# Optimization experiments

Measured on AMD Instinct MI355X. Metric: run time of the kernel, lower is better.

The kernel has to match this reference:

```python
import jax, jax.numpy as jnp
import numpy as np

HIDDEN = 2048
N_HEADS = 32
N_KV_HEADS = 8
HEAD_DIM = HIDDEN // N_HEADS  # 64
GROUPS = N_HEADS // N_KV_HEADS  # 4
ROPE_THETA = 10000.0
B, S = 1, 2048


def setup_inputs() -> dict:
    key = jax.random.key(0)
    ks = jax.random.split(key, 5)
    scale = 1.0 / np.sqrt(HIDDEN)
    return {
        "hidden_states": jax.random.normal(ks[0], (B, S, HIDDEN), dtype=jnp.float32),
        "Wq": jax.random.normal(ks[1], (HIDDEN, N_HEADS * HEAD_DIM), dtype=jnp.float32) * scale,
        "Wk": jax.random.normal(ks[2], (HIDDEN, N_KV_HEADS * HEAD_DIM), dtype=jnp.float32) * scale,
        "Wv": jax.random.normal(ks[3], (HIDDEN, N_KV_HEADS * HEAD_DIM), dtype=jnp.float32) * scale,
        "Wo": jax.random.normal(ks[4], (N_HEADS * HEAD_DIM, HIDDEN), dtype=jnp.float32) * scale,
    }


def _rope_tables(seq_len, dtype):
    # freqs_cos/sin buffers: [seq_len, HEAD_DIM//2]
    inv_freq = 1.0 / (ROPE_THETA ** (jnp.arange(0, HEAD_DIM, 2, dtype=jnp.float32) / HEAD_DIM))
    t = jnp.arange(seq_len, dtype=jnp.float32)
    freqs = jnp.outer(t, inv_freq)
    return jnp.cos(freqs).astype(dtype), jnp.sin(freqs).astype(dtype)


def _apply_rope(x, cos, sin):
    # x: [B, H, S, Dh], interleaved even/odd rotation
    xe = x[..., 0::2]
    xo = x[..., 1::2]
    # cos/sin: [S, Dh/2] -> broadcast over batch & heads
    out_e = xe * cos - xo * sin
    out_o = xe * sin + xo * cos
    return jnp.stack([out_e, out_o], axis=-1).reshape(x.shape)


def reference(hidden_states, Wq, Wk, Wv, Wo):
    bsz, q_len, _ = hidden_states.shape
    dtype = hidden_states.dtype

    q = (hidden_states @ Wq).reshape(bsz, q_len, N_HEADS, HEAD_DIM).transpose(0, 2, 1, 3)
    k = (hidden_states @ Wk).reshape(bsz, q_len, N_KV_HEADS, HEAD_DIM).transpose(0, 2, 1, 3)
    v = (hidden_states @ Wv).reshape(bsz, q_len, N_KV_HEADS, HEAD_DIM).transpose(0, 2, 1, 3)

    cos, sin = _rope_tables(q_len, dtype)
    q = _apply_rope(q, cos, sin)
    k = _apply_rope(k, cos, sin)

    # GQA: repeat_interleave kv heads to match query heads
    k = jnp.repeat(k, GROUPS, axis=1)  # [B, H, S, Dh]
    v = jnp.repeat(v, GROUPS, axis=1)

    # attention_mask=None path: no mask applied (matches module default)
    scores = jnp.einsum("bhqd,bhkd->bhqk", q, k) / jnp.sqrt(jnp.asarray(HEAD_DIM, dtype))
    attn = jax.nn.softmax(scores.astype(jnp.float32), axis=-1).astype(dtype)
    out = jnp.einsum("bhqk,bhkd->bhqd", attn, v)
    out = out.transpose(0, 2, 1, 3).reshape(bsz, q_len, N_HEADS * HEAD_DIM)
    return out @ Wo
```

## Files before the change

### kernel.cpp

```cpp
#include <hip/hip_runtime.h>

typedef __bf16 bf16x8 __attribute__((ext_vector_type(8)));
typedef float f32x4 __attribute__((ext_vector_type(4)));
typedef unsigned short u16x4 __attribute__((ext_vector_type(4)));
typedef unsigned short u16x8 __attribute__((ext_vector_type(8)));
typedef unsigned int u32x4 __attribute__((ext_vector_type(4)));

__device__ __forceinline__ float bf2f(unsigned short h) {
    union { unsigned int u; float f; } v;
    v.u = ((unsigned int)h) << 16;
    return v.f;
}
__device__ __forceinline__ unsigned short f2bf(float f) {
    return __builtin_bit_cast(unsigned short, (__bf16)f);
}
__device__ __forceinline__ void glds16(const unsigned short* g, unsigned short* l) {
    __builtin_amdgcn_global_load_lds((__attribute__((address_space(1))) void*)g,
                                     (__attribute__((address_space(3))) void*)l,
                                     16, 0, 0);
}

#define MFMA16(a, b, c) __builtin_amdgcn_mfma_f32_16x16x32_bf16((a), (b), (c), 0, 0, 0)

__global__ __launch_bounds__(256) void cvt_f32_bf16(const float* __restrict__ src,
                                                    unsigned short* __restrict__ dst) {
    const int i = (blockIdx.x * 256 + threadIdx.x) * 4;
    const float4 v = *(const float4*)(src + i);
    u16x4 o;
    o[0] = f2bf(v.x); o[1] = f2bf(v.y); o[2] = f2bf(v.z); o[3] = f2bf(v.w);
    *(u16x4*)(dst + i) = o;
}

__global__ __launch_bounds__(256) void cvt_transpose_wqkv(const float* __restrict__ Wq,
                                                          const float* __restrict__ Wk,
                                                          const float* __restrict__ Wv,
                                                          unsigned short* __restrict__ dst) {
    const int kb = blockIdx.x * 32;
    const int nb = blockIdx.y * 32;
    const float* src; int scol; int sld;
    if (nb < 2048)      { src = Wq; scol = nb;        sld = 2048; }
    else if (nb < 2560) { src = Wk; scol = nb - 2048; sld = 512;  }
    else                { src = Wv; scol = nb - 2560; sld = 512;  }
    __shared__ __align__(16) unsigned short tile[32][33];
    const int tx = threadIdx.x;
    const int ty = threadIdx.y;
#pragma unroll
    for (int i = 0; i < 32; i += 8)
        tile[ty + i][tx] = f2bf(src[(size_t)(kb + ty + i) * sld + (scol + tx)]);
    __syncthreads();
#pragma unroll
    for (int i = 0; i < 32; i += 8)
        dst[(size_t)(nb + ty + i) * 2048 + (kb + tx)] = tile[tx][ty + i];
}

__global__ __launch_bounds__(256) void cvt_transpose_f32(const float* __restrict__ src,
                                                         unsigned short* __restrict__ dst,
                                                         int sld, int dld) {
    __shared__ __align__(16) unsigned short tile[32][33];
    const int bx = blockIdx.x * 32;
    const int by = blockIdx.y * 32;
    const int tx = threadIdx.x;
    const int ty = threadIdx.y;
#pragma unroll
    for (int i = 0; i < 32; i += 8)
        tile[ty + i][tx] = f2bf(src[(size_t)(by + ty + i) * sld + (bx + tx)]);
    __syncthreads();
#pragma unroll
    for (int i = 0; i < 32; i += 8)
        dst[(size_t)(bx + ty + i) * dld + (by + tx)] = tile[tx][ty + i];
}

__global__ __launch_bounds__(256) void transpose_bf16(const unsigned short* __restrict__ src,
                                                      unsigned short* __restrict__ dst,
                                                      int sld, int dld) {
    __shared__ __align__(16) unsigned short tile[32][33];
    const int bx = blockIdx.x * 32;
    const int by = blockIdx.y * 32;
    const int tx = threadIdx.x;
    const int ty = threadIdx.y;
#pragma unroll
    for (int i = 0; i < 32; i += 8)
        tile[ty + i][tx] = src[(size_t)(by + ty + i) * sld + (bx + tx)];
    __syncthreads();
#pragma unroll
    for (int i = 0; i < 32; i += 8)
        dst[(size_t)(bx + ty + i) * dld + (by + tx)] = tile[tx][ty + i];
}

__global__ __launch_bounds__(256) void rope_k(unsigned short* __restrict__ qkv) {
    const int idx = blockIdx.x * 256 + threadIdx.x;
    const int s = idx / 1280;
    const int p = idx % 1280;
    const int head = p >> 5;
    const int i = p & 31;
    const size_t base = (size_t)s * 3072 + head * 64 + 2 * i;
    const float inv = exp2f(-0.41524101186092036f * (float)i);
    const float ang = (float)s * inv;
    float sn, cs;
    __sincosf(ang, &sn, &cs);
    const float xe = bf2f(qkv[base]);
    const float xo = bf2f(qkv[base + 1]);
    qkv[base]     = f2bf(xe * cs - xo * sn);
    qkv[base + 1] = f2bf(xe * sn + xo * cs);
}

template <int BM>
__global__ __launch_bounds__(256) void gemm_bt(const unsigned short* __restrict__ A,
                                               const unsigned short* __restrict__ BT,
                                               void* __restrict__ Cv,
                                               int K, int lda, int ldb, int ldc,
                                               int out_f32) {
    constexpr int MT = BM / 32;
    __shared__ __align__(16) unsigned short As[BM * 64];
    __shared__ __align__(16) unsigned short Bs[128 * 64];

    const int tid = threadIdx.x;
    const int lane = tid & 63;
    const int wave = tid >> 6;
    const int quad = lane >> 4;
    const int l15 = lane & 15;
    const int bm = blockIdx.x * BM;
    const int bn = blockIdx.y * 128;
    const int wm = (wave & 1) * (BM / 2);
    const int wn = (wave >> 1) * 64;

    const int srow = wave * 8 + (lane >> 3);
    const int sw = (lane & 7) ^ (srow & 7);
    const unsigned short* Ag = A + (size_t)(bm + srow) * lda + sw * 8;
    const unsigned short* Bg = BT + (size_t)(bn + srow) * ldb + sw * 8;
    unsigned short* Asl = As + wave * 512;
    unsigned short* Bsl = Bs + wave * 512;

    f32x4 acc[MT][4] = {};

    for (int k0 = 0; k0 < K; k0 += 64) {
#pragma unroll
        for (int i = 0; i < MT; i++)
            glds16(Ag + (size_t)(32 * i) * lda + k0, Asl + i * 2048);
#pragma unroll
        for (int i = 0; i < 4; i++)
            glds16(Bg + (size_t)(32 * i) * ldb + k0, Bsl + i * 2048);
        __syncthreads();
#pragma unroll
        for (int ks = 0; ks < 2; ks++) {
            bf16x8 af[MT], bfr[4];
#pragma unroll
            for (int mt = 0; mt < MT; mt++) {
                const int row = wm + 16 * mt + l15;
                af[mt] = __builtin_bit_cast(bf16x8,
                    *(const u32x4*)&As[row * 64 + (((quad + 4 * ks) ^ (row & 7)) * 8)]);
            }
#pragma unroll
            for (int nt = 0; nt < 4; nt++) {
                const int row = wn + 16 * nt + l15;
                bfr[nt] = __builtin_bit_cast(bf16x8,
                    *(const u32x4*)&Bs[row * 64 + (((quad + 4 * ks) ^ (row & 7)) * 8)]);
            }
#pragma unroll
            for (int mt = 0; mt < MT; mt++)
#pragma unroll
                for (int nt = 0; nt < 4; nt++)
                    acc[mt][nt] = MFMA16(af[mt], bfr[nt], acc[mt][nt]);
        }
        __syncthreads();
    }

#pragma unroll
    for (int mt = 0; mt < MT; mt++) {
#pragma unroll
        for (int nt = 0; nt < 4; nt++) {
#pragma unroll
            for (int r = 0; r < 4; r++) {
                const int row = bm + wm + 16 * mt + quad * 4 + r;
                const int col = bn + wn + 16 * nt + l15;
                if (out_f32)
                    ((float*)Cv)[(size_t)row * ldc + col] = acc[mt][nt][r];
                else
                    ((unsigned short*)Cv)[(size_t)row * ldc + col] = f2bf(acc[mt][nt][r]);
            }
        }
    }
}

__global__ __launch_bounds__(256) void attn_kernel(const unsigned short* __restrict__ qkv,
                                                   const unsigned short* __restrict__ vt,
                                                   unsigned short* __restrict__ attn_out) {
    const int qb = blockIdx.x;
    const int h = blockIdx.y;
    const int kvh = h >> 2;
    const int tid = threadIdx.x;
    const int lane = tid & 63;
    const int wave = tid >> 6;
    const int quad = lane >> 4;
    const int l15 = lane & 15;
    const int w0 = qb * 128 + wave * 32;

    __shared__ __align__(16) unsigned short Ks[64 * 64];
    __shared__ __align__(16) unsigned short Vs[64 * 64];
    __shared__ __align__(16) unsigned short Pl[4][32][72];
    unsigned short (*Pw)[72] = Pl[wave];

    const int srow = wave * 8 + (lane >> 3);
    const int sw = (lane & 7) ^ (srow & 7);
    const unsigned short* Kg = qkv + 2048 + kvh * 64 + sw * 8;
    const unsigned short* Vg = vt + (size_t)(kvh * 64 + srow) * 2048 + sw * 8;
    unsigned short* Ksl = Ks + wave * 512;
    unsigned short* Vsl = Vs + wave * 512;

    bf16x8 qf[2][2];
#pragma unroll
    for (int mt = 0; mt < 2; mt++)
#pragma unroll
        for (int ks = 0; ks < 2; ks++) {
            u32x4 raw = *(const u32x4*)&qkv[(size_t)(w0 + 16 * mt + l15) * 3072 + h * 64 + quad * 8 + 32 * ks];
            u16x8 t = __builtin_bit_cast(u16x8, raw);
#pragma unroll
            for (int j = 0; j < 8; j++) t[j] = f2bf(bf2f(t[j]) * 0.125f);
            qf[mt][ks] = __builtin_bit_cast(bf16x8, t);
        }

    float l_part[2][4] = {};
    f32x4 acc_o[2][4] = {};

    const float LOG2E = 1.44269504088896f;
    const float MB = -17.3123404906676f;

    for (int kb = 0; kb < 32; kb++) {
        const int kbase = kb * 64;

#pragma unroll
        for (int i = 0; i < 2; i++) {
            glds16(Kg + (size_t)(kbase + srow + 32 * i) * 3072, Ksl + i * 2048);
            glds16(Vg + (size_t)(32 * i) * 2048 + kbase, Vsl + i * 2048);
        }
        __syncthreads();

        f32x4 s[2][4] = {};
#pragma unroll
        for (int n = 0; n < 4; n++) {
            const int row = 16 * n + l15;
            const bf16x8 kf0 = __builtin_bit_cast(bf16x8,
                *(const u32x4*)&Ks[row * 64 + ((quad ^ (l15 & 7)) * 8)]);
            const bf16x8 kf1 = __builtin_bit_cast(bf16x8,
                *(const u32x4*)&Ks[row * 64 + (((quad + 4) ^ (l15 & 7)) * 8)]);
#pragma unroll
            for (int mt = 0; mt < 2; mt++) {
                s[mt][n] = MFMA16(qf[mt][0], kf0, s[mt][n]);
                s[mt][n] = MFMA16(qf[mt][1], kf1, s[mt][n]);
            }
        }

#pragma unroll
        for (int mt = 0; mt < 2; mt++)
#pragma unroll
            for (int n = 0; n < 4; n++)
#pragma unroll
                for (int r = 0; r < 4; r++) {
                    const float p = exp2f(fmaf(s[mt][n][r], LOG2E, MB));
                    l_part[mt][r] += p;
                    Pw[16 * mt + quad * 4 + r][16 * n + l15] = f2bf(p);
                }

        bf16x8 pf[2][2];
#pragma unroll
        for (int mt = 0; mt < 2; mt++) {
            pf[mt][0] = __builtin_bit_cast(bf16x8, *(const u32x4*)&Pw[16 * mt + l15][quad * 8]);
            pf[mt][1] = __builtin_bit_cast(bf16x8, *(const u32x4*)&Pw[16 * mt + l15][quad * 8 + 32]);
        }

#pragma unroll
        for (int nt = 0; nt < 4; nt++) {
            const int row = 16 * nt + l15;
            const bf16x8 vf0 = __builtin_bit_cast(bf16x8,
                *(const u32x4*)&Vs[row * 64 + ((quad ^ (l15 & 7)) * 8)]);
            const bf16x8 vf1 = __builtin_bit_cast(bf16x8,
                *(const u32x4*)&Vs[row * 64 + (((quad + 4) ^ (l15 & 7)) * 8)]);
#pragma unroll
            for (int mt = 0; mt < 2; mt++) {
                acc_o[mt][nt] = MFMA16(pf[mt][0], vf0, acc_o[mt][nt]);
                acc_o[mt][nt] = MFMA16(pf[mt][1], vf1, acc_o[mt][nt]);
            }
        }
        __syncthreads();
    }

#pragma unroll
    for (int off = 1; off < 16; off <<= 1)
#pragma unroll
        for (int mt = 0; mt < 2; mt++)
#pragma unroll
            for (int r = 0; r < 4; r++)
                l_part[mt][r] += __shfl_xor(l_part[mt][r], off, 64);

#pragma unroll
    for (int mt = 0; mt < 2; mt++) {
        float linv[4];
#pragma unroll
        for (int r = 0; r < 4; r++) linv[r] = 1.0f / l_part[mt][r];
#pragma unroll
        for (int nt = 0; nt < 4; nt++)
#pragma unroll
            for (int r = 0; r < 4; r++)
                attn_out[(size_t)(w0 + 16 * mt + quad * 4 + r) * 2048 + h * 64 + 16 * nt + l15] =
                    f2bf(acc_o[mt][nt][r] * linv[r]);
    }
}

extern "C" void kernel_launch(void* const* d_in, const int* in_sizes, int n_in,
                              void* d_out, int out_size, void* d_ws, size_t ws_size,
                              hipStream_t stream) {
    (void)in_sizes; (void)n_in; (void)out_size; (void)ws_size;

    const float* X  = (const float*)d_in[0];
    const float* Wq = (const float*)d_in[1];
    const float* Wk = (const float*)d_in[2];
    const float* Wv = (const float*)d_in[3];
    const float* Wo = (const float*)d_in[4];

    unsigned short* ws16  = (unsigned short*)d_ws;
    unsigned short* Xbf   = ws16;
    unsigned short* wqkvT = ws16 + (size_t)4194304;
    unsigned short* qkv   = (unsigned short*)d_out;
    unsigned short* vt    = ws16;
    unsigned short* attnO = ws16 + (size_t)1048576;
    unsigned short* woT   = ws16 + (size_t)5242880;

    const dim3 tb(32, 8);

    cvt_f32_bf16<<<4096, 256, 0, stream>>>(X, Xbf);
    cvt_transpose_wqkv<<<dim3(64, 96), tb, 0, stream>>>(Wq, Wk, Wv, wqkvT);

    gemm_bt<64><<<dim3(32, 24), 256, 0, stream>>>(Xbf, wqkvT, qkv, 2048, 2048, 2048, 3072, 0);

    rope_k<<<dim3((2048 * 1280) / 256), 256, 0, stream>>>(qkv);

    transpose_bf16<<<dim3(16, 64), tb, 0, stream>>>(qkv + 2560, vt, 3072, 2048);
    cvt_transpose_f32<<<dim3(64, 64), tb, 0, stream>>>(Wo, woT, 2048, 2048);

    attn_kernel<<<dim3(16, 32), 256, 0, stream>>>(qkv, vt, attnO);

    gemm_bt<64><<<dim3(32, 16), 256, 0, stream>>>(attnO, woT, (void*)d_out, 2048, 2048, 2048, 2048, 1);
}
```

Baseline: 260.6 us.

## Fuse prep kernels, fold RoPE into QKV GEMM epilogue, widen attention KV tile

Merges the X/weight conversion kernels into one launch and the Wo/V transposes into another. RoPE is applied in the QKV GEMM epilogue using a lane shuffle to fetch the even/odd partner, which removes a separate read-modify-write pass over Q and K. The attention kernel now processes 128 keys per barrier, and S is computed transposed so P is stored to LDS as packed 4-element vectors with simpler row-sum reduction. This cuts launch count and barriers, but uses more LDS per block and adds sincos work to the GEMM epilogue.

```diff
diff --git a/kernel.cpp b/kernel.cpp
--- a/kernel.cpp
+++ b/kernel.cpp
@@ -22,89 +22,73 @@
 
 #define MFMA16(a, b, c) __builtin_amdgcn_mfma_f32_16x16x32_bf16((a), (b), (c), 0, 0, 0)
 
-__global__ __launch_bounds__(256) void cvt_f32_bf16(const float* __restrict__ src,
-                                                    unsigned short* __restrict__ dst) {
-    const int i = (blockIdx.x * 256 + threadIdx.x) * 4;
-    const float4 v = *(const float4*)(src + i);
-    u16x4 o;
-    o[0] = f2bf(v.x); o[1] = f2bf(v.y); o[2] = f2bf(v.z); o[3] = f2bf(v.w);
-    *(u16x4*)(dst + i) = o;
-}
-
-__global__ __launch_bounds__(256) void cvt_transpose_wqkv(const float* __restrict__ Wq,
-                                                          const float* __restrict__ Wk,
-                                                          const float* __restrict__ Wv,
-                                                          unsigned short* __restrict__ dst) {
-    const int kb = blockIdx.x * 32;
-    const int nb = blockIdx.y * 32;
-    const float* src; int scol; int sld;
+__global__ __launch_bounds__(256) void prep1(const float* __restrict__ X,
+                                             const float* __restrict__ Wq,
+                                             const float* __restrict__ Wk,
+                                             const float* __restrict__ Wv,
+                                             unsigned short* __restrict__ Xbf,
+                                             unsigned short* __restrict__ wqkvT) {
+    const int b = blockIdx.x;
+    const int tid = threadIdx.x;
+    if (b < 4096) {
+        const int i = (b * 256 + tid) * 4;
+        const float4 v = *(const float4*)(X + i);
+        u16x4 o;
+        o[0] = f2bf(v.x); o[1] = f2bf(v.y); o[2] = f2bf(v.z); o[3] = f2bf(v.w);
+        *(u16x4*)(Xbf + i) = o;
+        return;
+    }
+    __shared__ __align__(16) unsigned short tile[32][33];
+    const int tx = tid & 31, ty = tid >> 5;
+    const int b2 = b - 4096;
+    const int kb = (b2 & 63) * 32;
+    const int nb = (b2 >> 6) * 32;
+    const float* src; int scol, sld;
     if (nb < 2048)      { src = Wq; scol = nb;        sld = 2048; }
     else if (nb < 2560) { src = Wk; scol = nb - 2048; sld = 512;  }
     else                { src = Wv; scol = nb - 2560; sld = 512;  }
-    __shared__ __align__(16) unsigned short tile[32][33];
-    const int tx = threadIdx.x;
-    const int ty = threadIdx.y;
 #pragma unroll
     for (int i = 0; i < 32; i += 8)
         tile[ty + i][tx] = f2bf(src[(size_t)(kb + ty + i) * sld + (scol + tx)]);
     __syncthreads();
 #pragma unroll
     for (int i = 0; i < 32; i += 8)
-        dst[(size_t)(nb + ty + i) * 2048 + (kb + tx)] = tile[tx][ty + i];
-}
-
-__global__ __launch_bounds__(256) void cvt_transpose_f32(const float* __restrict__ src,
-                                                         unsigned short* __restrict__ dst,
-                                                         int sld, int dld) {
+        wqkvT[(size_t)(nb + ty + i) * 2048 + (kb + tx)] = tile[tx][ty + i];
+}
+
+__global__ __launch_bounds__(256) void prep2(const float* __restrict__ Wo,
+                                             const unsigned short* __restrict__ qkv,
+                                             unsigned short* __restrict__ woT,
+                                             unsigned short* __restrict__ vt) {
+    const int b = blockIdx.x;
+    const int tid = threadIdx.x;
+    const int tx = tid & 31, ty = tid >> 5;
     __shared__ __align__(16) unsigned short tile[32][33];
-    const int bx = blockIdx.x * 32;
-    const int by = blockIdx.y * 32;
-    const int tx = threadIdx.x;
-    const int ty = threadIdx.y;
-#pragma unroll
-    for (int i = 0; i < 32; i += 8)
-        tile[ty + i][tx] = f2bf(src[(size_t)(by + ty + i) * sld + (bx + tx)]);
-    __syncthreads();
-#pragma unroll
-    for (int i = 0; i < 32; i += 8)
-        dst[(size_t)(bx + ty + i) * dld + (by + tx)] = tile[tx][ty + i];
-}
-
-__global__ __launch_bounds__(256) void transpose_bf16(const unsigned short* __restrict__ src,
-                                                      unsigned short* __restrict__ dst,
-                                                      int sld, int dld) {
-    __shared__ __align__(16) unsigned short tile[32][33];
-    const int bx = blockIdx.x * 32;
-    const int by = blockIdx.y * 32;
-    const int tx = threadIdx.x;
-    const int ty = threadIdx.y;
-#pragma unroll
-    for (int i = 0; i < 32; i += 8)
-        tile[ty + i][tx] = src[(size_t)(by + ty + i) * sld + (bx + tx)];
-    __syncthreads();
-#pragma unroll
-    for (int i = 0; i < 32; i += 8)
-        dst[(size_t)(bx + ty + i) * dld + (by + tx)] = tile[tx][ty + i];
-}
-
-__global__ __launch_bounds__(256) void rope_k(unsigned short* __restrict__ qkv) {
-    const int idx = blockIdx.x * 256 + threadIdx.x;
-    const int s = idx / 1280;
-    const int p = idx % 1280;
-    const int head = p >> 5;
-    const int i = p & 31;
-    const size_t base = (size_t)s * 3072 + head * 64 + 2 * i;
-    const float inv = exp2f(-0.41524101186092036f * (float)i);
-    const float ang = (float)s * inv;
-    float sn, cs;
-    __sincosf(ang, &sn, &cs);
-    const float xe = bf2f(qkv[base]);
-    const float xo = bf2f(qkv[base + 1]);
-    qkv[base]     = f2bf(xe * cs - xo * sn);
-    qkv[base + 1] = f2bf(xe * sn + xo * cs);
-}
-
-template <int BM>
+    if (b < 4096) {
+        const int kb = (b & 63) * 32;
+        const int nb = (b >> 6) * 32;
+#pragma unroll
+        for (int i = 0; i < 32; i += 8)
+            tile[ty + i][tx] = f2bf(Wo[(size_t)(kb + ty + i) * 2048 + (nb + tx)]);
+        __syncthreads();
+#pragma unroll
+        for (int i = 0; i < 32; i += 8)
+            woT[(size_t)(nb + ty + i) * 2048 + (kb + tx)] = tile[tx][ty + i];
+    } else {
+        const int b2 = b - 4096;
+        const int bx = (b2 & 15) * 32;
+        const int by = (b2 >> 4) * 32;
+#pragma unroll
+        for (int i = 0; i < 32; i += 8)
+            tile[ty + i][tx] = qkv[(size_t)(by + ty + i) * 3072 + 2560 + bx + tx];
+        __syncthreads();
+#pragma unroll
+        for (int i = 0; i < 32; i += 8)
+            vt[(size_t)(bx + ty + i) * 2048 + (by + tx)] = tile[tx][ty + i];
+    }
+}
+
+template <int BM, bool ROPE>
 __global__ __launch_bounds__(256) void gemm_bt(const unsigned short* __restrict__ A,
                                                const unsigned short* __restrict__ BT,
                                                void* __restrict__ Cv,
@@ -163,6 +147,29 @@
                     acc[mt][nt] = MFMA16(af[mt], bfr[nt], acc[mt][nt]);
         }
         __syncthreads();
+    }
+
+    if (ROPE) {
+#pragma unroll
+        for (int mt = 0; mt < MT; mt++) {
+#pragma unroll
+            for (int nt = 0; nt < 4; nt++) {
+                const int col = bn + wn + 16 * nt + l15;
+                if (col < 2560) {
+                    const int i = (col & 63) >> 1;
+                    const float inv = exp2f(-0.41524101186092036f * (float)i);
+                    const float sign = (col & 1) ? 1.0f : -1.0f;
+#pragma unroll
+                    for (int r = 0; r < 4; r++) {
+                        const int row = bm + wm + 16 * mt + quad * 4 + r;
+                        float sn, cs;
+                        __sincosf((float)row * inv, &sn, &cs);
+                        const float partner = __shfl_xor(acc[mt][nt][r], 1, 64);
+                        acc[mt][nt][r] = acc[mt][nt][r] * cs + sign * partner * sn;
+                    }
+                }
+            }
+        }
     }
 
 #pragma unroll
@@ -195,16 +202,18 @@
     const int l15 = lane & 15;
     const int w0 = qb * 128 + wave * 32;
 
-    __shared__ __align__(16) unsigned short Ks[64 * 64];
-    __shared__ __align__(16) unsigned short Vs[64 * 64];
-    __shared__ __align__(16) unsigned short Pl[4][32][72];
-    unsigned short (*Pw)[72] = Pl[wave];
+    __shared__ __align__(16) unsigned short Ks[128 * 64];
+    __shared__ __align__(16) unsigned short Vs[64 * 128];
+    __shared__ __align__(16) unsigned short St[4][32][72];
+    unsigned short (*Sw)[72] = St[wave];
 
     const int srow = wave * 8 + (lane >> 3);
-    const int sw = (lane & 7) ^ (srow & 7);
-    const unsigned short* Kg = qkv + 2048 + kvh * 64 + sw * 8;
-    const unsigned short* Vg = vt + (size_t)(kvh * 64 + srow) * 2048 + sw * 8;
+    const int swK = (lane & 7) ^ (srow & 7);
+    const unsigned short* Kg = qkv + 2048 + kvh * 64 + swK * 8;
     unsigned short* Ksl = Ks + wave * 512;
+    const int vrow = wave * 4 + (lane >> 4);
+    const int swV = (lane & 15) ^ (vrow & 7);
+    const unsigned short* Vg = vt + (size_t)(kvh * 64 + vrow) * 2048 + swV * 8;
     unsigned short* Vsl = Vs + wave * 512;
 
     bf16x8 qf[2][2];
@@ -219,84 +228,88 @@
             qf[mt][ks] = __builtin_bit_cast(bf16x8, t);
         }
 
-    float l_part[2][4] = {};
+    float l_part[2] = {};
     f32x4 acc_o[2][4] = {};
 
     const float LOG2E = 1.44269504088896f;
     const float MB = -17.3123404906676f;
 
-    for (int kb = 0; kb < 32; kb++) {
-        const int kbase = kb * 64;
-
-#pragma unroll
-        for (int i = 0; i < 2; i++) {
+    for (int kb2 = 0; kb2 < 16; kb2++) {
+        const int kbase = kb2 * 128;
+#pragma unroll
+        for (int i = 0; i < 4; i++) {
             glds16(Kg + (size_t)(kbase + srow + 32 * i) * 3072, Ksl + i * 2048);
-            glds16(Vg + (size_t)(32 * i) * 2048 + kbase, Vsl + i * 2048);
-        }
-        __syncthreads();
-
-        f32x4 s[2][4] = {};
-#pragma unroll
-        for (int n = 0; n < 4; n++) {
-            const int row = 16 * n + l15;
-            const bf16x8 kf0 = __builtin_bit_cast(bf16x8,
-                *(const u32x4*)&Ks[row * 64 + ((quad ^ (l15 & 7)) * 8)]);
-            const bf16x8 kf1 = __builtin_bit_cast(bf16x8,
-                *(const u32x4*)&Ks[row * 64 + (((quad + 4) ^ (l15 & 7)) * 8)]);
+            glds16(Vg + (size_t)(16 * i) * 2048 + kbase, Vsl + i * 2048);
+        }
+        __syncthreads();
+
+#pragma unroll
+        for (int kh = 0; kh < 2; kh++) {
+            f32x4 st[2][4] = {};
+#pragma unroll
+            for (int n = 0; n < 4; n++) {
+                const int row = kh * 64 + 16 * n + l15;
+                const bf16x8 kf0 = __builtin_bit_cast(bf16x8,
+                    *(const u32x4*)&Ks[row * 64 + ((quad ^ (l15 & 7)) * 8)]);
+                const bf16x8 kf1 = __builtin_bit_cast(bf16x8,
+                    *(const u32x4*)&Ks[row * 64 + (((quad + 4) ^ (l15 & 7)) * 8)]);
+#pragma unroll
+                for (int mt = 0; mt < 2; mt++) {
+                    st[mt][n] = MFMA16(kf0, qf[mt][0], st[mt][n]);
+                    st[mt][n] = MFMA16(kf1, qf[mt][1], st[mt][n]);
+                }
+            }
+
+#pragma unroll
+            for (int mt = 0; mt < 2; mt++)
+#pragma unroll
+                for (int n = 0; n < 4; n++) {
+                    u16x4 pk;
+#pragma unroll
+                    for (int r = 0; r < 4; r++) {
+                        const float p = exp2f(fmaf(st[mt][n][r], LOG2E, MB));
+                        l_part[mt] += p;
+                        pk[r] = f2bf(p);
+                    }
+                    *(u16x4*)&Sw[16 * mt + l15][16 * n + quad * 4] = pk;
+                }
+
+            bf16x8 pf[2][2];
 #pragma unroll
             for (int mt = 0; mt < 2; mt++) {
-                s[mt][n] = MFMA16(qf[mt][0], kf0, s[mt][n]);
-                s[mt][n] = MFMA16(qf[mt][1], kf1, s[mt][n]);
-            }
-        }
-
-#pragma unroll
-        for (int mt = 0; mt < 2; mt++)
-#pragma unroll
-            for (int n = 0; n < 4; n++)
-#pragma unroll
-                for (int r = 0; r < 4; r++) {
-                    const float p = exp2f(fmaf(s[mt][n][r], LOG2E, MB));
-                    l_part[mt][r] += p;
-                    Pw[16 * mt + quad * 4 + r][16 * n + l15] = f2bf(p);
+                pf[mt][0] = __builtin_bit_cast(bf16x8, *(const u32x4*)&Sw[16 * mt + l15][quad * 8]);
+                pf[mt][1] = __builtin_bit_cast(bf16x8, *(const u32x4*)&Sw[16 * mt + l15][quad * 8 + 32]);
+            }
+
+#pragma unroll
+            for (int nt = 0; nt < 4; nt++) {
+                const int row = 16 * nt + l15;
+                const int c0 = kh * 8 + (quad ^ (l15 & 7));
+                const int c1 = kh * 8 + ((quad + 4) ^ (l15 & 7));
+                const bf16x8 vf0 = __builtin_bit_cast(bf16x8, *(const u32x4*)&Vs[row * 128 + c0 * 8]);
+                const bf16x8 vf1 = __builtin_bit_cast(bf16x8, *(const u32x4*)&Vs[row * 128 + c1 * 8]);
+#pragma unroll
+                for (int mt = 0; mt < 2; mt++) {
+                    acc_o[mt][nt] = MFMA16(pf[mt][0], vf0, acc_o[mt][nt]);
+                    acc_o[mt][nt] = MFMA16(pf[mt][1], vf1, acc_o[mt][nt]);
                 }
-
-        bf16x8 pf[2][2];
-#pragma unroll
-        for (int mt = 0; mt < 2; mt++) {
-            pf[mt][0] = __builtin_bit_cast(bf16x8, *(const u32x4*)&Pw[16 * mt + l15][quad * 8]);
-            pf[mt][1] = __builtin_bit_cast(bf16x8, *(const u32x4*)&Pw[16 * mt + l15][quad * 8 + 32]);
-        }
-
-#pragma unroll
-        for (int nt = 0; nt < 4; nt++) {
-            const int row = 16 * nt + l15;
-            const bf16x8 vf0 = __builtin_bit_cast(bf16x8,
-                *(const u32x4*)&Vs[row * 64 + ((quad ^ (l15 & 7)) * 8)]);
-            const bf16x8 vf1 = __builtin_bit_cast(bf16x8,
-                *(const u32x4*)&Vs[row * 64 + (((quad + 4) ^ (l15 & 7)) * 8)]);
-#pragma unroll
-            for (int mt = 0; mt < 2; mt++) {
-                acc_o[mt][nt] = MFMA16(pf[mt][0], vf0, acc_o[mt][nt]);
-                acc_o[mt][nt] = MFMA16(pf[mt][1], vf1, acc_o[mt][nt]);
-            }
-        }
-        __syncthreads();
-    }
-
-#pragma unroll
-    for (int off = 1; off < 16; off <<= 1)
-#pragma unroll
-        for (int mt = 0; mt < 2; mt++)
-#pragma unroll
-            for (int r = 0; r < 4; r++)
-                l_part[mt][r] += __shfl_xor(l_part[mt][r], off, 64);
+            }
+        }
+        __syncthreads();
+    }
+
+#pragma unroll
+    for (int mt = 0; mt < 2; mt++) {
+        l_part[mt] += __shfl_xor(l_part[mt], 16, 64);
+        l_part[mt] += __shfl_xor(l_part[mt], 32, 64);
+    }
 
 #pragma unroll
     for (int mt = 0; mt < 2; mt++) {
         float linv[4];
 #pragma unroll
-        for (int r = 0; r < 4; r++) linv[r] = 1.0f / l_part[mt][r];
+        for (int r = 0; r < 4; r++)
+            linv[r] = 1.0f / __shfl(l_part[mt], quad * 4 + r, 64);
 #pragma unroll
         for (int nt = 0; nt < 4; nt++)
 #pragma unroll
@@ -325,19 +338,13 @@
     unsigned short* attnO = ws16 + (size_t)1048576;
     unsigned short* woT   = ws16 + (size_t)5242880;
 
-    const dim3 tb(32, 8);
-
-    cvt_f32_bf16<<<4096, 256, 0, stream>>>(X, Xbf);
-    cvt_transpose_wqkv<<<dim3(64, 96), tb, 0, stream>>>(Wq, Wk, Wv, wqkvT);
-
-    gemm_bt<64><<<dim3(32, 24), 256, 0, stream>>>(Xbf, wqkvT, qkv, 2048, 2048, 2048, 3072, 0);
-
-    rope_k<<<dim3((2048 * 1280) / 256), 256, 0, stream>>>(qkv);
-
-    transpose_bf16<<<dim3(16, 64), tb, 0, stream>>>(qkv + 2560, vt, 3072, 2048);
-    cvt_transpose_f32<<<dim3(64, 64), tb, 0, stream>>>(Wo, woT, 2048, 2048);
+    prep1<<<10240, 256, 0, stream>>>(X, Wq, Wk, Wv, Xbf, wqkvT);
+
+    gemm_bt<64, true><<<dim3(32, 24), 256, 0, stream>>>(Xbf, wqkvT, qkv, 2048, 2048, 2048, 3072, 0);
+
+    prep2<<<5120, 256, 0, stream>>>(Wo, qkv, woT, vt);
 
     attn_kernel<<<dim3(16, 32), 256, 0, stream>>>(qkv, vt, attnO);
 
-    gemm_bt<64><<<dim3(32, 16), 256, 0, stream>>>(attnO, woT, (void*)d_out, 2048, 2048, 2048, 2048, 1);
-}
+    gemm_bt<64, false><<<dim3(32, 16), 256, 0, stream>>>(attnO, woT, (void*)d_out, 2048, 2048, 2048, 2048, 1);
+}
```

Measured after the change: 242.6 us. -6.9%, faster.
